# Performance work log

Hardware: AMD Instinct MI355X
Metric: run time of the kernel (lower is better)

Reference implementation:

```python
import jax, jax.numpy as jnp
import numpy as np

D = 1024
H = 16
HD = D // H  # 64

def setup_inputs() -> dict:
    key = jax.random.key(0)
    ks = jax.random.split(key, 7)
    B, S = 2, 2048
    x = jax.random.normal(ks[0], (B, S, D), dtype=jnp.float32)
    M = jax.random.randint(ks[1], (B, S, S), 0, 2, dtype=jnp.int32)
    s = 1.0 / np.sqrt(D)
    W_q = jax.random.normal(ks[2], (D, D), dtype=jnp.float32) * s
    W_k = jax.random.normal(ks[3], (D, D), dtype=jnp.float32) * s
    W_v = jax.random.normal(ks[4], (D, D), dtype=jnp.float32) * s
    W_o = jax.random.normal(ks[5], (D, D), dtype=jnp.float32) * s
    b_o = jax.random.normal(ks[6], (D,), dtype=jnp.float32) * 0.01
    return {"x": x, "M": M, "W_q": W_q, "W_k": W_k, "W_v": W_v, "W_o": W_o, "b_o": b_o}

def reference(x, M, W_q, W_k, W_v, W_o, b_o):
    B, S, _ = x.shape
    scale = HD ** -0.5
    # project and split heads: [B, H, S, HD]
    def heads(W):
        return (x @ W.T).reshape(B, S, H, HD).transpose(0, 2, 1, 3)
    Q, K, V = heads(W_q), heads(W_k), heads(W_v)
    scores = jnp.einsum('bhqd,bhkd->bhqk', Q, K) * scale
    mask = (M[:, None, :, :] == 0)  # broadcast over heads
    scores = jnp.where(mask, jnp.float32(-1e9), scores)
    A = jax.nn.softmax(scores, axis=-1)
    out = jnp.einsum('bhqk,bhkd->bhqd', A, V)
    out = out.transpose(0, 2, 1, 3).reshape(B, S, D)
    return out @ W_o.T + b_o
```

## Files before the change

### kernel.cpp

```cpp
#include <hip/hip_runtime.h>
#include <hip/hip_bf16.h>

typedef unsigned short u16;
typedef unsigned int u32;
typedef unsigned long long u64;
typedef _Float16 f16;
typedef __attribute__((__ext_vector_type__(4))) _Float16 f16x4;
typedef __attribute__((__ext_vector_type__(8))) short bf16x8;
typedef __attribute__((__ext_vector_type__(4))) float f32x4;
typedef __attribute__((__ext_vector_type__(16))) float f32x16;
typedef __attribute__((__ext_vector_type__(2))) int i32x2;

__device__ __forceinline__ u16 f2bf(float f) {
    u32 u = __float_as_uint(f);
    return (u16)((u + 0x7fffu + ((u >> 16) & 1u)) >> 16);
}

__global__ __launch_bounds__(256) void prep_kernel(
    const float4* __restrict__ x,  const float4* __restrict__ wq,
    const float4* __restrict__ wk, const float4* __restrict__ wv,
    const float4* __restrict__ wo,
    u16* __restrict__ xb, u16* __restrict__ wqb, u16* __restrict__ wkb,
    u16* __restrict__ wvb, u16* __restrict__ wob,
    const int* __restrict__ M, u64* __restrict__ Mb2)
{
    if (blockIdx.x < 2048) {
        #pragma unroll
        for (int it = 0; it < 4; it++) {
            int gid = it * 524288 + blockIdx.x * 256 + threadIdx.x;
            const float4* src; u16* dst; int off;
            if (gid < 1048576) { src = x; dst = xb; off = gid; }
            else {
                int g = gid - 1048576;
                int sel = g >> 18;
                off = g & 262143;
                src = sel == 0 ? wq : sel == 1 ? wk : sel == 2 ? wv : wo;
                dst = sel == 0 ? wqb : sel == 1 ? wkb : sel == 2 ? wvb : wob;
            }
            float4 f = src[off];
            ushort4 o;
            o.x = f2bf(f.x); o.y = f2bf(f.y); o.z = f2bf(f.z); o.w = f2bf(f.w);
            ((ushort4*)dst)[off] = o;
        }
    } else {
        int wg   = (blockIdx.x - 2048) * 4 + (threadIdx.x >> 6);
        int lane = threadIdx.x & 63;
        int q     = wg & 2047;
        int wquad = (wg >> 11) & 7;
        int b     = wg >> 14;
        size_t base = ((size_t)(b * 2048 + q)) * 2048 + wquad * 256 + lane;
        #pragma unroll
        for (int i = 0; i < 4; i++) {
            u64 bits = __ballot(M[base + i * 64] != 0);
            if (lane == 0)
                Mb2[(size_t)(b * 32 + wquad * 4 + i) * 2048 + q] = bits;
        }
    }
}

template<int MODE, int BN>
__global__ __launch_bounds__(256) void gemm_k(
    const u16* __restrict__ Ag, const u16* __restrict__ Bg,
    u16* __restrict__ Cq, u16* __restrict__ Kfr, u16* __restrict__ Vfr,
    float* __restrict__ Cf, const float* __restrict__ bias)
{
    constexpr int Kd = 1024;
    constexpr int NB = BN / 32;
    constexpr int BUF = 8192 + BN * 64;
    constexpr int GX = (MODE == 0) ? 24 : 16;
    constexpr int NWG = GX * 32;
    __shared__ u16 SM[2 * BUF];
    const int tid  = threadIdx.x;
    const int wave = tid >> 6, lane = tid & 63;
    const int quad = lane >> 4, l16 = lane & 15;

    int flat = blockIdx.y * GX + blockIdx.x;
    flat = (flat & 7) * (NWG >> 3) + (flat >> 3);
    const int n0 = (flat % GX) * BN;
    const int m0 = (flat / GX) * 128;

    const int wm = (wave & 1) * 64, wn = (wave >> 1) * (BN / 2);
    f32x4 acc[4][NB];
    #pragma unroll
    for (int i = 0; i < 4; i++)
        #pragma unroll
        for (int j = 0; j < NB; j++)
            acc[i][j] = (f32x4){0.f, 0.f, 0.f, 0.f};

    const int sr = lane >> 2;
    const int sk = (lane & 3) * 8;
    const int ca0 = wave * 2, ca1 = ca0 + 1;
    const u16* gA0 = Ag + (size_t)(m0 + ca0 * 16 + sr) * Kd + sk;
    const u16* gA1 = Ag + (size_t)(m0 + ca1 * 16 + sr) * Kd + sk;
    const int cb0 = (BN == 128) ? wave * 2 : wave;
    const u16* gB0 = Bg + (size_t)(n0 + cb0 * 16 + sr) * Kd + sk;
    const u16* gB1 = (BN == 128) ? Bg + (size_t)(n0 + (cb0 + 1) * 16 + sr) * Kd + sk : nullptr;

    #define GLL16(gp, lp) __builtin_amdgcn_global_load_lds( \
        (const __attribute__((address_space(1))) void*)(gp), \
        (__attribute__((address_space(3))) void*)(lp), 16, 0, 0)

    #define STAGE(K0, BASE)                                            \
    {                                                                  \
        u16* As0_ = (BASE);                                            \
        u16* As1_ = (BASE) + 4096;                                     \
        u16* Bs0_ = (BASE) + 8192;                                     \
        u16* Bs1_ = (BASE) + 8192 + BN * 32;                           \
        GLL16(gA0 + (K0), As0_ + ca0 * 512);                           \
        GLL16(gA1 + (K0), As0_ + ca1 * 512);                           \
        GLL16(gB0 + (K0), Bs0_ + cb0 * 512);                           \
        if (BN == 128) GLL16(gB1 + (K0), Bs0_ + (cb0 + 1) * 512);      \
        GLL16(gA0 + (K0) + 32, As1_ + ca0 * 512);                      \
        GLL16(gA1 + (K0) + 32, As1_ + ca1 * 512);                      \
        GLL16(gB0 + (K0) + 32, Bs1_ + cb0 * 512);                      \
        if (BN == 128) GLL16(gB1 + (K0) + 32, Bs1_ + (cb0 + 1) * 512); \
    }

    STAGE(0, SM);
    __syncthreads();

    for (int k0 = 0; k0 < Kd; k0 += 64) {
        u16* cur = SM + ((k0 >> 6) & 1) * BUF;
        u16* nxt = SM + (((k0 >> 6) & 1) ^ 1) * BUF;
        if (k0 + 64 < Kd) STAGE(k0 + 64, nxt);

        #pragma unroll
        for (int kk = 0; kk < 2; kk++) {
            const u16* Ah = cur + (kk ? 4096 : 0);
            const u16* Bh = cur + 8192 + (kk ? BN * 32 : 0);
            bf16x8 af[4], bfr[NB];
            #pragma unroll
            for (int mb = 0; mb < 4; mb++)
                af[mb] = *(const bf16x8*)&Ah[(wm + mb * 16 + l16) * 32 + quad * 8];
            #pragma unroll
            for (int nb = 0; nb < NB; nb++)
                bfr[nb] = *(const bf16x8*)&Bh[(wn + nb * 16 + l16) * 32 + quad * 8];
            #pragma unroll
            for (int mb = 0; mb < 4; mb++)
                #pragma unroll
                for (int nb = 0; nb < NB; nb++)
                    acc[mb][nb] = __builtin_amdgcn_mfma_f32_16x16x32_bf16(
                        af[mb], bfr[nb], acc[mb][nb], 0, 0, 0);
        }
        __syncthreads();
    }
    #undef STAGE
    #undef GLL16

    if (MODE == 1) {
        float* OT = (float*)SM;
        #pragma unroll
        for (int mb = 0; mb < 4; mb++)
            #pragma unroll
            for (int nb = 0; nb < NB; nb++) {
                const int rowb = wm + mb * 16 + quad * 4;
                const int colb = wn + nb * 16 + l16;
                const float bv = bias[n0 + colb];
                #pragma unroll
                for (int r = 0; r < 4; r++)
                    OT[(rowb + r) * 68 + colb] = acc[mb][nb][r] + bv;
            }
        __syncthreads();
        #pragma unroll
        for (int it = 0; it < 8; it++) {
            const int g = (it * 256 + tid) * 4;
            const int row = g >> 6, col = g & 63;
            *(f32x4*)(Cf + (size_t)(m0 + row) * 1024 + n0 + col) =
                *(const f32x4*)(OT + row * 68 + col);
        }
        return;
    }

    const int region = n0 >> 10;
    if (region == 0) {
        u16* QT = SM;
        #pragma unroll
        for (int mb = 0; mb < 4; mb++)
            #pragma unroll
            for (int nb = 0; nb < NB; nb++) {
                const int rowb = wm + mb * 16 + quad * 4;
                const int colb = wn + nb * 16 + l16;
                #pragma unroll
                for (int r = 0; r < 4; r++)
                    QT[(rowb + r) * 132 + colb] =
                        f2bf(acc[mb][nb][r] * 0.18033688011112042f);
            }
        __syncthreads();
        #pragma unroll
        for (int it = 0; it < 8; it++) {
            const int g = (it * 256 + tid) * 8;
            const int row = g >> 7, col = g & 127;
            *(bf16x8*)(Cq + (size_t)(m0 + row) * 1024 + (n0 & 1023) + col) =
                *(const bf16x8*)(QT + row * 132 + col);
        }
        return;
    }

    const int bb = m0 >> 11;
    const int kt_base = (m0 & 2047) >> 6;
    const int head_base = (n0 & 1023) >> 6;
    u16* dst = (region == 1) ? Kfr : Vfr;
    #pragma unroll
    for (int pass = 0; pass < 2; pass++) {
        __syncthreads();
        #pragma unroll
        for (int mb = 0; mb < 4; mb++) {
            const int rowb = wm + mb * 16 + quad * 4;
            if ((rowb >> 6) != pass) continue;
            #pragma unroll
            for (int nb = 0; nb < NB; nb++) {
                const int ccol = wn + nb * 16 + l16;
                const int h2 = ccol >> 6, dd = ccol & 63;
                if (region == 1) {
                    const int t = dd >> 4, hik = (dd >> 3) & 1, j = dd & 7;
                    #pragma unroll
                    for (int r = 0; r < 4; r++) {
                        const int km = (rowb + r) & 63;
                        const int f = (km >> 5) * 4 + t;
                        const int lanek = hik * 32 + (km & 31);
                        SM[((h2 * 8 + f) * 64 + lanek) * 8 + j] = f2bf(acc[mb][nb][r]);
                    }
                } else {
                    const int kinb = rowb & 63;
                    const int t = kinb >> 4, hiv = (kinb >> 3) & 1, jb = kinb & 7;
                    const int f = (dd >> 5) * 4 + t;
                    const int lanev = hiv * 32 + (dd & 31);
                    ushort4 pk;
                    pk.x = f2bf(acc[mb][nb][0]); pk.y = f2bf(acc[mb][nb][1]);
                    pk.z = f2bf(acc[mb][nb][2]); pk.w = f2bf(acc[mb][nb][3]);
                    *(ushort4*)&SM[((h2 * 8 + f) * 64 + lanev) * 8 + jb] = pk;
                }
            }
        }
        __syncthreads();
        const int h2g = tid >> 7;
        const int inner = (tid & 127) * 32;
        const size_t gbase =
            ((size_t)(bb * 16 + head_base + h2g) * 32 + kt_base + pass) * 4096;
        #pragma unroll
        for (int c = 0; c < 4; c++)
            *(bf16x8*)&dst[gbase + inner + c * 8] =
                *(const bf16x8*)&SM[h2g * 4096 + inner + c * 8];
    }
}

__global__ __launch_bounds__(256, 2) void attn_kernel(
    const u16* __restrict__ Qg, const u16* __restrict__ Kfr, const u16* __restrict__ Vfr,
    const u64* __restrict__ Mb2, u16* __restrict__ AO)
{
    int flat = (blockIdx.z * 16 + blockIdx.y) * 16 + blockIdx.x;
    flat = (flat & 7) * 64 + (flat >> 3);
    const int qt = flat & 15;
    const int h  = (flat >> 4) & 15;
    const int b  = flat >> 8;
    const int tid = threadIdx.x, wave = tid >> 6, lane = tid & 63;
    const int l31 = lane & 31, hi = lane >> 5;
    const int pair = wave >> 1;
    const int kh   = wave & 1;

    const int qrow0 = qt * 128 + pair * 64;
    const int bh    = b * 16 + h;

    bf16x8 qfa[4], qfb[4];
    {
        const u16* qp = Qg + ((size_t)b * 2048 + qrow0 + l31) * 1024 + h * 64 + hi * 8;
        #pragma unroll
        for (int t = 0; t < 4; t++) qfa[t] = *(const bf16x8*)(qp + t * 16);
        #pragma unroll
        for (int t = 0; t < 4; t++) qfb[t] = *(const bf16x8*)(qp + 32 * 1024 + t * 16);
    }

    const u32 fro = (u32)bh * 131072u + (u32)lane * 8u;
    const u64* mp = Mb2 + (size_t)(b * 32) * 2048 + qrow0 + l31;

    bf16x8 ones;
    #pragma unroll
    for (int j = 0; j < 8; j++) ones[j] = (short)0x3F80;

    f32x16 oa0, oa1, ob0, ob1, la, lb;
    #pragma unroll
    for (int i = 0; i < 16; i++) {
        oa0[i] = 0.f; oa1[i] = 0.f; ob0[i] = 0.f; ob1[i] = 0.f;
        la[i] = 0.f;  lb[i] = 0.f;
    }

    const int kt0 = kh * 16;
    #pragma unroll 1
    for (int kt = kt0; kt < kt0 + 16; ++kt) {
        const u64 mwa = mp[(size_t)kt * 2048];
        const u64 mwb = mp[(size_t)kt * 2048 + 32];
        const u32 fb = fro + (u32)kt * 4096u;

        #pragma unroll
        for (int ph = 0; ph < 2; ph++) {
            bf16x8 kf[4], vf[4];
            #pragma unroll
            for (int t = 0; t < 4; t++)
                kf[t] = *(const bf16x8*)(Kfr + fb + (u32)(ph * 4 + t) * 512u);
            vf[0] = *(const bf16x8*)(Vfr + fb + (u32)(2 * ph) * 512u);
            vf[1] = *(const bf16x8*)(Vfr + fb + (u32)(2 * ph + 1) * 512u);
            vf[2] = *(const bf16x8*)(Vfr + fb + (u32)(4 + 2 * ph) * 512u);
            vf[3] = *(const bf16x8*)(Vfr + fb + (u32)(4 + 2 * ph + 1) * 512u);

            const u32 mna = ~((ph ? (u32)(mwa >> 32) : (u32)mwa) >> (hi * 4));
            const u32 mnb = ~((ph ? (u32)(mwb >> 32) : (u32)mwb) >> (hi * 4));
            f32x16 sa, sb;
            #pragma unroll
            for (int reg = 0; reg < 16; reg++) {
                const int kb2 = (reg & 3) + 8 * (reg >> 2);
                sa[reg] = __int_as_float(
                    __builtin_amdgcn_sbfe((int)mna, kb2, 1) & (int)0xFF800000);
                sb[reg] = __int_as_float(
                    __builtin_amdgcn_sbfe((int)mnb, kb2, 1) & (int)0xFF800000);
            }
            __builtin_amdgcn_s_setprio(1);
            #pragma unroll
            for (int t = 0; t < 4; t++) {
                sa = __builtin_amdgcn_mfma_f32_32x32x16_bf16(kf[t], qfa[t], sa, 0, 0, 0);
                sb = __builtin_amdgcn_mfma_f32_32x32x16_bf16(kf[t], qfb[t], sb, 0, 0, 0);
            }
            __builtin_amdgcn_s_setprio(0);

            u32 wa[8], wb[8];
            #pragma unroll
            for (int i = 0; i < 8; i++) {
                const float ea0 = __builtin_amdgcn_exp2f(sa[2 * i]);
                const float ea1 = __builtin_amdgcn_exp2f(sa[2 * i + 1]);
                wa[i] = __builtin_amdgcn_perm(__float_as_uint(ea1),
                                              __float_as_uint(ea0), 0x07060302u);
                const float eb0 = __builtin_amdgcn_exp2f(sb[2 * i]);
                const float eb1 = __builtin_amdgcn_exp2f(sb[2 * i + 1]);
                wb[i] = __builtin_amdgcn_perm(__float_as_uint(eb1),
                                              __float_as_uint(eb0), 0x07060302u);
            }

            bf16x8 pba[2], pbb[2];
            #pragma unroll
            for (int fl = 0; fl < 2; fl++) {
                i32x2 a02 = __builtin_amdgcn_permlane32_swap(
                    (int)wa[4 * fl + 0], (int)wa[4 * fl + 2], false, false);
                i32x2 a13 = __builtin_amdgcn_permlane32_swap(
                    (int)wa[4 * fl + 1], (int)wa[4 * fl + 3], false, false);
                union { u32 u[4]; bf16x8 v; } fa;
                fa.u[0] = (u32)a02[0]; fa.u[1] = (u32)a13[0];
                fa.u[2] = (u32)a02[1]; fa.u[3] = (u32)a13[1];
                pba[fl] = fa.v;
                i32x2 b02 = __builtin_amdgcn_permlane32_swap(
                    (int)wb[4 * fl + 0], (int)wb[4 * fl + 2], false, false);
                i32x2 b13 = __builtin_amdgcn_permlane32_swap(
                    (int)wb[4 * fl + 1], (int)wb[4 * fl + 3], false, false);
                union { u32 u[4]; bf16x8 v; } fbu;
                fbu.u[0] = (u32)b02[0]; fbu.u[1] = (u32)b13[0];
                fbu.u[2] = (u32)b02[1]; fbu.u[3] = (u32)b13[1];
                pbb[fl] = fbu.v;
            }

            __builtin_amdgcn_s_setprio(1);
            oa0 = __builtin_amdgcn_mfma_f32_32x32x16_bf16(vf[0], pba[0], oa0, 0, 0, 0);
            ob0 = __builtin_amdgcn_mfma_f32_32x32x16_bf16(vf[0], pbb[0], ob0, 0, 0, 0);
            oa0 = __builtin_amdgcn_mfma_f32_32x32x16_bf16(vf[1], pba[1], oa0, 0, 0, 0);
            ob0 = __builtin_amdgcn_mfma_f32_32x32x16_bf16(vf[1], pbb[1], ob0, 0, 0, 0);
            oa1 = __builtin_amdgcn_mfma_f32_32x32x16_bf16(vf[2], pba[0], oa1, 0, 0, 0);
            ob1 = __builtin_amdgcn_mfma_f32_32x32x16_bf16(vf[2], pbb[0], ob1, 0, 0, 0);
            oa1 = __builtin_amdgcn_mfma_f32_32x32x16_bf16(vf[3], pba[1], oa1, 0, 0, 0);
            ob1 = __builtin_amdgcn_mfma_f32_32x32x16_bf16(vf[3], pbb[1], ob1, 0, 0, 0);
            la  = __builtin_amdgcn_mfma_f32_32x32x16_bf16(ones,  pba[0], la,  0, 0, 0);
            lb  = __builtin_amdgcn_mfma_f32_32x32x16_bf16(ones,  pbb[0], lb,  0, 0, 0);
            la  = __builtin_amdgcn_mfma_f32_32x32x16_bf16(ones,  pba[1], la,  0, 0, 0);
            lb  = __builtin_amdgcn_mfma_f32_32x32x16_bf16(ones,  pbb[1], lb,  0, 0, 0);
            __builtin_amdgcn_s_setprio(0);
        }
    }

    __shared__ float MRG[2 * 64 * 68];
    float* slot = &MRG[(pair * 64 + lane) * 68];
    if (kh == 1) {
        #pragma unroll
        for (int i = 0; i < 4; i++) {
            *(f32x4*)(slot +      4 * i) = (f32x4){oa0[4*i], oa0[4*i+1], oa0[4*i+2], oa0[4*i+3]};
            *(f32x4*)(slot + 16 + 4 * i) = (f32x4){oa1[4*i], oa1[4*i+1], oa1[4*i+2], oa1[4*i+3]};
            *(f32x4*)(slot + 32 + 4 * i) = (f32x4){ob0[4*i], ob0[4*i+1], ob0[4*i+2], ob0[4*i+3]};
            *(f32x4*)(slot + 48 + 4 * i) = (f32x4){ob1[4*i], ob1[4*i+1], ob1[4*i+2], ob1[4*i+3]};
        }
        slot[64] = la[0];
        slot[65] = lb[0];
    }
    __syncthreads();
    if (kh == 0) {
        #pragma unroll
        for (int i = 0; i < 16; i++) {
            oa0[i] += slot[i];
            oa1[i] += slot[16 + i];
            ob0[i] += slot[32 + i];
            ob1[i] += slot[48 + i];
        }
        const float invA = 1.0f / (la[0] + slot[64]);
        const float invB = 1.0f / (lb[0] + slot[65]);
        const size_t qbase = ((size_t)b * 2048 + qrow0 + l31) * 1024 + h * 64;
        #pragma unroll
        for (int tile = 0; tile < 2; tile++) {
            #pragma unroll
            for (int g = 0; g < 4; g++) {
                const int d0 = tile * 32 + g * 8 + hi * 4;
                ushort4 pa, pb;
                #pragma unroll
                for (int r = 0; r < 4; r++) {
                    const int reg = g * 4 + r;
                    const float va = (tile == 0 ? oa0[reg] : oa1[reg]) * invA;
                    const float vb = (tile == 0 ? ob0[reg] : ob1[reg]) * invB;
                    ((u16*)&pa)[r] = f2bf(va);
                    ((u16*)&pb)[r] = f2bf(vb);
                }
                *(ushort4*)&AO[qbase + d0] = pa;
                *(ushort4*)&AO[qbase + (size_t)32 * 1024 + d0] = pb;
            }
        }
    }
}

extern "C" void kernel_launch(void* const* d_in, const int* in_sizes, int n_in,
                              void* d_out, int out_size, void* d_ws, size_t ws_size,
                              hipStream_t stream)
{
    const float* x  = (const float*)d_in[0];
    const int*   Mm = (const int*)d_in[1];
    const float* Wq = (const float*)d_in[2];
    const float* Wk = (const float*)d_in[3];
    const float* Wv = (const float*)d_in[4];
    const float* Wo = (const float*)d_in[5];
    const float* bo = (const float*)d_in[6];
    float* out = (float*)d_out;

    u16* ws  = (u16*)d_ws;
    u16* xb  = ws;
    u16* wqb = xb  + 4194304;
    u16* wkb = wqb + 1048576;
    u16* wvb = wkb + 1048576;
    u16* wob = wvb + 1048576;
    u16* Qb  = wob + 1048576;
    u16* Kfr = Qb  + 4194304;
    u16* Vfr = Kfr + 4194304;
    u16* AOb = Vfr + 4194304;
    u64* Mb2 = (u64*)(AOb + 4194304);

    prep_kernel<<<10240, 256, 0, stream>>>(
        (const float4*)x, (const float4*)Wq, (const float4*)Wk,
        (const float4*)Wv, (const float4*)Wo, xb, wqb, wkb, wvb, wob,
        Mm, Mb2);

    dim3 g1(24, 32, 1);
    gemm_k<0, 128><<<g1, 256, 0, stream>>>(xb, wqb, Qb, Kfr, Vfr, nullptr, nullptr);

    dim3 g2(16, 16, 2);
    attn_kernel<<<g2, 256, 0, stream>>>(Qb, Kfr, Vfr, Mb2, AOb);

    dim3 g3(16, 32, 1);
    gemm_k<1, 64><<<g3, 256, 0, stream>>>(AOb, wob, nullptr, nullptr, nullptr,
                                          out, bo);
}
```

Measured before the change: 211.2 us.

## Split attention key range four ways per block and merge partials in fp16 LDS

After: 578.9 us. +174.0%, slower.

```diff
diff --git a/kernel.cpp b/kernel.cpp
--- a/kernel.cpp
+++ b/kernel.cpp
@@ -244,21 +244,20 @@
     }
 }
 
-__global__ __launch_bounds__(256, 2) void attn_kernel(
+__global__ __launch_bounds__(256, 4) void attn_kernel(
     const u16* __restrict__ Qg, const u16* __restrict__ Kfr, const u16* __restrict__ Vfr,
     const u64* __restrict__ Mb2, u16* __restrict__ AO)
 {
-    int flat = (blockIdx.z * 16 + blockIdx.y) * 16 + blockIdx.x;
-    flat = (flat & 7) * 64 + (flat >> 3);
-    const int qt = flat & 15;
-    const int h  = (flat >> 4) & 15;
-    const int b  = flat >> 8;
+    int flat = (blockIdx.z * 16 + blockIdx.y) * 32 + blockIdx.x;
+    flat = (flat & 7) * 128 + (flat >> 3);
+    const int qt = flat & 31;
+    const int h  = (flat >> 5) & 15;
+    const int b  = flat >> 9;
     const int tid = threadIdx.x, wave = tid >> 6, lane = tid & 63;
     const int l31 = lane & 31, hi = lane >> 5;
-    const int pair = wave >> 1;
-    const int kh   = wave & 1;
-
-    const int qrow0 = qt * 128 + pair * 64;
+    const int kh = wave;
+
+    const int qrow0 = qt * 64;
     const int bh    = b * 16 + h;
 
     bf16x8 qfa[4], qfb[4];
@@ -284,9 +283,9 @@
         la[i] = 0.f;  lb[i] = 0.f;
     }
 
-    const int kt0 = kh * 16;
+    const int kt0 = kh * 8;
     #pragma unroll 1
-    for (int kt = kt0; kt < kt0 + 16; ++kt) {
+    for (int kt = kt0; kt < kt0 + 8; ++kt) {
         const u64 mwa = mp[(size_t)kt * 2048];
         const u64 mwb = mp[(size_t)kt * 2048 + 32];
         const u32 fb = fro + (u32)kt * 4096u;
@@ -372,30 +371,53 @@
         }
     }
 
-    __shared__ float MRG[2 * 64 * 68];
-    float* slot = &MRG[(pair * 64 + lane) * 68];
-    if (kh == 1) {
+    __shared__ f16   MRGv[3][64][68];
+    __shared__ float MRGl[3][64][2];
+    if (kh != 0) {
+        f16* vp = &MRGv[kh - 1][lane][0];
         #pragma unroll
         for (int i = 0; i < 4; i++) {
-            *(f32x4*)(slot +      4 * i) = (f32x4){oa0[4*i], oa0[4*i+1], oa0[4*i+2], oa0[4*i+3]};
-            *(f32x4*)(slot + 16 + 4 * i) = (f32x4){oa1[4*i], oa1[4*i+1], oa1[4*i+2], oa1[4*i+3]};
-            *(f32x4*)(slot + 32 + 4 * i) = (f32x4){ob0[4*i], ob0[4*i+1], ob0[4*i+2], ob0[4*i+3]};
-            *(f32x4*)(slot + 48 + 4 * i) = (f32x4){ob1[4*i], ob1[4*i+1], ob1[4*i+2], ob1[4*i+3]};
-        }
-        slot[64] = la[0];
-        slot[65] = lb[0];
+            f16x4 p0, p1, p2, p3;
+            #pragma unroll
+            for (int r = 0; r < 4; r++) {
+                p0[r] = (f16)oa0[4 * i + r];
+                p1[r] = (f16)oa1[4 * i + r];
+                p2[r] = (f16)ob0[4 * i + r];
+                p3[r] = (f16)ob1[4 * i + r];
+            }
+            *(f16x4*)(vp +      4 * i) = p0;
+            *(f16x4*)(vp + 16 + 4 * i) = p1;
+            *(f16x4*)(vp + 32 + 4 * i) = p2;
+            *(f16x4*)(vp + 48 + 4 * i) = p3;
+        }
+        MRGl[kh - 1][lane][0] = la[0];
+        MRGl[kh - 1][lane][1] = lb[0];
     }
     __syncthreads();
     if (kh == 0) {
-        #pragma unroll
-        for (int i = 0; i < 16; i++) {
-            oa0[i] += slot[i];
-            oa1[i] += slot[16 + i];
-            ob0[i] += slot[32 + i];
-            ob1[i] += slot[48 + i];
-        }
-        const float invA = 1.0f / (la[0] + slot[64]);
-        const float invB = 1.0f / (lb[0] + slot[65]);
+        float lA = la[0], lB = lb[0];
+        #pragma unroll
+        for (int s = 0; s < 3; s++) {
+            const f16* vp = &MRGv[s][lane][0];
+            #pragma unroll
+            for (int i = 0; i < 4; i++) {
+                f16x4 v0 = *(const f16x4*)(vp +      4 * i);
+                f16x4 v1 = *(const f16x4*)(vp + 16 + 4 * i);
+                f16x4 v2 = *(const f16x4*)(vp + 32 + 4 * i);
+                f16x4 v3 = *(const f16x4*)(vp + 48 + 4 * i);
+                #pragma unroll
+                for (int r = 0; r < 4; r++) {
+                    oa0[4 * i + r] += (float)v0[r];
+                    oa1[4 * i + r] += (float)v1[r];
+                    ob0[4 * i + r] += (float)v2[r];
+                    ob1[4 * i + r] += (float)v3[r];
+                }
+            }
+            lA += MRGl[s][lane][0];
+            lB += MRGl[s][lane][1];
+        }
+        const float invA = 1.0f / lA;
+        const float invB = 1.0f / lB;
         const size_t qbase = ((size_t)b * 2048 + qrow0 + l31) * 1024 + h * 64;
         #pragma unroll
         for (int tile = 0; tile < 2; tile++) {
@@ -451,7 +473,7 @@
     dim3 g1(24, 32, 1);
     gemm_k<0, 128><<<g1, 256, 0, stream>>>(xb, wqb, Qb, Kfr, Vfr, nullptr, nullptr);
 
-    dim3 g2(16, 16, 2);
+    dim3 g2(32, 16, 2);
     attn_kernel<<<g2, 256, 0, stream>>>(Qb, Kfr, Vfr, Mb2, AOb);
 
     dim3 g3(16, 32, 1);
```
